# Kernel optimization log

Measured on AMD Instinct MI355X. Metric: run time of the kernel, lower is better.

## Reference

```python
import jax, jax.numpy as jnp
import numpy as np

STRIDES = (4.0, 8.0, 16.0, 32.0)
IMG = 1024.0


def setup_inputs() -> dict:
    key = jax.random.key(0)
    ks = jax.random.split(key, 10)
    N, P = 512, 128
    feat0 = jax.random.normal(ks[0], (2, 256, 256, 256), jnp.float32)
    feat1 = jax.random.normal(ks[1], (2, 256, 128, 128), jnp.float32)
    feat2 = jax.random.normal(ks[2], (2, 256, 64, 64), jnp.float32)
    feat3 = jax.random.normal(ks[3], (2, 256, 32, 32), jnp.float32)
    b = jax.random.randint(ks[4], (N,), 0, 2).astype(jnp.float32)
    x1 = jax.random.uniform(ks[5], (N,)) * 512.0
    y1 = jax.random.uniform(ks[6], (N,)) * 512.0
    w = 16.0 + jax.random.uniform(ks[7], (N,)) * 496.0
    h = 16.0 + jax.random.uniform(ks[8], (N,)) * 496.0
    rois = jnp.stack([b, x1, y1, x1 + w, y1 + h], axis=1)  # [N,5]
    points = jax.random.uniform(ks[9], (N, P, 2), jnp.float32)  # rel coords in [0,1]
    return {"feat0": feat0, "feat1": feat1, "feat2": feat2, "feat3": feat3,
            "rois": rois, "points": points}


def _sample_level(feat, coords, batch_idx, stride):
    # feat: [B,C,H,W]; coords: [N,P,2] absolute image (x,y); -> [N,C,P]
    B, C, H, W = feat.shape
    # grid_sample align_corners=False: pixel coord = img_coord/stride - 0.5
    px = coords[..., 0] / stride - 0.5
    py = coords[..., 1] / stride - 0.5
    x0 = jnp.floor(px)
    y0 = jnp.floor(py)
    wx = px - x0  # weight of x0+1
    wy = py - y0
    x0i = x0.astype(jnp.int32)
    y0i = y0.astype(jnp.int32)

    def gather(yi, xi):
        valid = (xi >= 0) & (xi < W) & (yi >= 0) & (yi < H)  # zeros padding
        xc = jnp.clip(xi, 0, W - 1)
        yc = jnp.clip(yi, 0, H - 1)
        v = feat[batch_idx[:, None], :, yc, xc]  # [N,P,C]
        return v * valid[..., None].astype(feat.dtype)

    v00 = gather(y0i, x0i)
    v01 = gather(y0i, x0i + 1)
    v10 = gather(y0i + 1, x0i)
    v11 = gather(y0i + 1, x0i + 1)
    wx = wx[..., None]
    wy = wy[..., None]
    out = (v00 * (1 - wx) * (1 - wy) + v01 * wx * (1 - wy)
           + v10 * (1 - wx) * wy + v11 * wx * wy)  # [N,P,C]
    return out.transpose(0, 2, 1)  # [N,C,P]


def reference(feat0, feat1, feat2, feat3, rois, points):
    batch_idx = rois[:, 0].astype(jnp.int32)  # [N]
    xy1 = rois[:, 1:3]  # [N,2]
    xy2 = rois[:, 3:5]
    # roi_point2img_coord: rel point -> absolute image coordinate
    coords = xy1[:, None, :] + points * (xy2 - xy1)[:, None, :]  # [N,P,2]
    feats = (feat0, feat1, feat2, feat3)
    per_level = [_sample_level(f, coords, batch_idx, s) for f, s in zip(feats, STRIDES)]
    return jnp.concatenate(per_level, axis=1)  # [N, sum(C)=1024, P]
```

## Files before the change

kernel.cpp:

```cpp
#include <hip/hip_runtime.h>
#include <hip/hip_bf16.h>

#define N_ROIS 512
#define P_PTS  128
#define C_CH   256
#define TILE_P 32

#define L0_OFS 0
#define L1_OFS 33554432u
#define L2_OFS 41943040u
#define L3_OFS 44040192u
#define WS_ELEMS_NEEDED 44564480u

__device__ inline unsigned pack_bf16x2(float lo, float hi) {
    __hip_bfloat162 h = __float22bfloat162_rn(make_float2(lo, hi));
    unsigned r;
    __builtin_memcpy(&r, &h, 4);
    return r;
}

__global__ __launch_bounds__(256) void transpose_all_bf16(
    const float* __restrict__ f0, const float* __restrict__ f1,
    const float* __restrict__ f2, const float* __restrict__ f3,
    unsigned short* __restrict__ ws)
{
    const float* in; unsigned short* outp; int HW, pt;
    const int px = blockIdx.x;
    if (px < 2048)      { in = f0; outp = ws + L0_OFS; HW = 65536; pt = px; }
    else if (px < 2560) { in = f1; outp = ws + L1_OFS; HW = 16384; pt = px - 2048; }
    else if (px < 2688) { in = f2; outp = ws + L2_OFS; HW = 4096;  pt = px - 2560; }
    else                { in = f3; outp = ws + L3_OFS; HW = 1024;  pt = px - 2688; }

    __shared__ float tile[32][33];
    const int pix0 = pt * 32;
    const int c0   = blockIdx.y * 32;
    const int b    = blockIdx.z;
    in   += (size_t)b * C_CH * HW;
    outp += (size_t)b * C_CH * HW;
    const int tx = threadIdx.x;
    const int ty = threadIdx.y;

    #pragma unroll
    for (int i = 0; i < 32; i += 8)
        tile[ty + i][tx] = in[(size_t)(c0 + ty + i) * HW + pix0 + tx];
    __syncthreads();

    const int tid2 = ty * 32 + tx;
    const int wpix = tid2 >> 3;
    const int wq   = tid2 & 7;
    uint2 pk;
    pk.x = pack_bf16x2(tile[wq * 4 + 0][wpix], tile[wq * 4 + 1][wpix]);
    pk.y = pack_bf16x2(tile[wq * 4 + 2][wpix], tile[wq * 4 + 3][wpix]);
    *((uint2*)(outp + (size_t)(pix0 + wpix) * C_CH + c0 + wq * 4)) = pk;
}

__global__ __launch_bounds__(256) void mpe_sample_nhwc_bf16_v4(
    const unsigned short* __restrict__ fT,
    const float* __restrict__ rois, const float* __restrict__ points,
    float* __restrict__ out)
{
    const int blk = blockIdx.x;
    const int n   = blk >> 2;
    const int lvl = blk & 3;

    int H; float inv_stride; size_t lofs;
    if      (lvl == 0) { H = 256; inv_stride = 0.25f;    lofs = L0_OFS; }
    else if (lvl == 1) { H = 128; inv_stride = 0.125f;   lofs = L1_OFS; }
    else if (lvl == 2) { H = 64;  inv_stride = 0.0625f;  lofs = L2_OFS; }
    else               { H = 32;  inv_stride = 0.03125f; lofs = L3_OFS; }
    const int W  = H;
    const int HW = H * W;
    const unsigned short* feat = fT + lofs;

    __shared__ int   s_off[P_PTS][4];
    __shared__ float s_w[P_PTS][4];
    __shared__ float s_t[TILE_P][C_CH];

    const int tid = threadIdx.x;

    if (tid < P_PTS) {
        const int p = tid;
        const float bx = rois[n * 5 + 0];
        const float x1 = rois[n * 5 + 1];
        const float y1 = rois[n * 5 + 2];
        const float x2 = rois[n * 5 + 3];
        const float y2 = rois[n * 5 + 4];
        const float ptx = points[(n * P_PTS + p) * 2 + 0];
        const float pty = points[(n * P_PTS + p) * 2 + 1];

        const float cx = x1 + ptx * (x2 - x1);
        const float cy = y1 + pty * (y2 - y1);
        const float px = cx * inv_stride - 0.5f;
        const float py = cy * inv_stride - 0.5f;
        const float x0f = floorf(px);
        const float y0f = floorf(py);
        const float wx = px - x0f;
        const float wy = py - y0f;
        const int x0 = (int)x0f;
        const int y0 = (int)y0f;
        const int base = (int)bx * HW;

        #pragma unroll
        for (int k = 0; k < 4; ++k) {
            const int xi = x0 + (k & 1);
            const int yi = y0 + (k >> 1);
            const bool valid = (xi >= 0) & (xi < W) & (yi >= 0) & (yi < H);
            const int xc = min(max(xi, 0), W - 1);
            const int yc = min(max(yi, 0), H - 1);
            const float wk = ((k & 1) ? wx : 1.0f - wx) *
                             ((k >> 1) ? wy : 1.0f - wy);
            s_off[p][k] = base + yc * W + xc;
            s_w[p][k]   = valid ? wk : 0.0f;
        }
    }
    __syncthreads();

    const int wave = tid >> 6;
    const int lane = tid & 63;

    uint2 v[8][4];
    #pragma unroll
    for (int j = 0; j < 8; ++j) {
        const int pp = wave * 8 + j;
        #pragma unroll
        for (int k = 0; k < 4; ++k)
            v[j][k] = *((const uint2*)(feat + (size_t)s_off[pp][k] * C_CH) + lane);
    }

    for (int tile = 0; tile < P_PTS / TILE_P; ++tile) {
        const int pbase = tile * TILE_P + wave * 8;

        #pragma unroll
        for (int j = 0; j < 8; ++j) {
            const int pp = pbase + j;
            float4 a = make_float4(0.f, 0.f, 0.f, 0.f);
            #pragma unroll
            for (int k = 0; k < 4; ++k) {
                const float wk = s_w[pp][k];
                a.x = fmaf(__uint_as_float(v[j][k].x << 16),         wk, a.x);
                a.y = fmaf(__uint_as_float(v[j][k].x & 0xffff0000u), wk, a.y);
                a.z = fmaf(__uint_as_float(v[j][k].y << 16),         wk, a.z);
                a.w = fmaf(__uint_as_float(v[j][k].y & 0xffff0000u), wk, a.w);
            }
            *((float4*)&s_t[wave * 8 + j][lane * 4]) = a;
        }
        __syncthreads();

        if (tile < P_PTS / TILE_P - 1) {
            #pragma unroll
            for (int j = 0; j < 8; ++j) {
                const int pp = pbase + TILE_P + j;
                #pragma unroll
                for (int k = 0; k < 4; ++k)
                    v[j][k] = *((const uint2*)(feat + (size_t)s_off[pp][k] * C_CH) + lane);
            }
        }

        float* ob = out + ((size_t)n * 1024 + (size_t)lvl * 256 + tid) * P_PTS
                        + tile * TILE_P;
        #pragma unroll
        for (int i = 0; i < TILE_P / 4; ++i) {
            float4 o = make_float4(s_t[i * 4 + 0][tid], s_t[i * 4 + 1][tid],
                                   s_t[i * 4 + 2][tid], s_t[i * 4 + 3][tid]);
            *((float4*)(ob + i * 4)) = o;
        }
        __syncthreads();
    }
}

__global__ __launch_bounds__(256) void mpe_sample_nchw(
    const float* __restrict__ feat0, const float* __restrict__ feat1,
    const float* __restrict__ feat2, const float* __restrict__ feat3,
    const float* __restrict__ rois,  const float* __restrict__ points,
    float* __restrict__ out)
{
    const int blk = blockIdx.x;
    const int n   = blk >> 2;
    const int lvl = blk & 3;

    const float* feat;
    int H; float inv_stride;
    if      (lvl == 0) { feat = feat0; H = 256; inv_stride = 0.25f;    }
    else if (lvl == 1) { feat = feat1; H = 128; inv_stride = 0.125f;   }
    else if (lvl == 2) { feat = feat2; H = 64;  inv_stride = 0.0625f;  }
    else               { feat = feat3; H = 32;  inv_stride = 0.03125f; }
    const int W  = H;
    const int HW = H * W;

    __shared__ int   s_off[4][P_PTS];
    __shared__ float s_w[4][P_PTS];
    const int tid = threadIdx.x;

    if (tid < P_PTS) {
        const int p = tid;
        const float bx = rois[n * 5 + 0];
        const float x1 = rois[n * 5 + 1];
        const float y1 = rois[n * 5 + 2];
        const float x2 = rois[n * 5 + 3];
        const float y2 = rois[n * 5 + 4];
        const float ptx = points[(n * P_PTS + p) * 2 + 0];
        const float pty = points[(n * P_PTS + p) * 2 + 1];
        const float cx = x1 + ptx * (x2 - x1);
        const float cy = y1 + pty * (y2 - y1);
        const float px = cx * inv_stride - 0.5f;
        const float py = cy * inv_stride - 0.5f;
        const float x0f = floorf(px);
        const float y0f = floorf(py);
        const float wx = px - x0f;
        const float wy = py - y0f;
        const int x0 = (int)x0f;
        const int y0 = (int)y0f;
        const int base = (int)bx * C_CH * HW;
        #pragma unroll
        for (int k = 0; k < 4; ++k) {
            const int xi = x0 + (k & 1);
            const int yi = y0 + (k >> 1);
            const bool valid = (xi >= 0) & (xi < W) & (yi >= 0) & (yi < H);
            const int xc = min(max(xi, 0), W - 1);
            const int yc = min(max(yi, 0), H - 1);
            const float wk = ((k & 1) ? wx : 1.0f - wx) *
                             ((k >> 1) ? wy : 1.0f - wy);
            s_off[k][p] = base + yc * W + xc;
            s_w[k][p]   = valid ? wk : 0.0f;
        }
    }
    __syncthreads();

    const int p  = tid & (P_PTS - 1);
    const int c0 = tid >> 7;
    const int   off0 = s_off[0][p], off1 = s_off[1][p],
                off2 = s_off[2][p], off3 = s_off[3][p];
    const float w0 = s_w[0][p], w1 = s_w[1][p],
                w2 = s_w[2][p], w3 = s_w[3][p];
    const float* p0 = feat + off0 + c0 * HW;
    const float* p1 = feat + off1 + c0 * HW;
    const float* p2 = feat + off2 + c0 * HW;
    const float* p3 = feat + off3 + c0 * HW;
    float* po = out + ((size_t)n * 1024 + (size_t)lvl * 256 + c0) * P_PTS + p;
    const int step = 2 * HW;
    #pragma unroll 4
    for (int pass = 0; pass < C_CH / 2; ++pass) {
        *po = p0[0] * w0 + p1[0] * w1 + p2[0] * w2 + p3[0] * w3;
        p0 += step; p1 += step; p2 += step; p3 += step;
        po += 2 * P_PTS;
    }
}

extern "C" void kernel_launch(void* const* d_in, const int* in_sizes, int n_in,
                              void* d_out, int out_size, void* d_ws, size_t ws_size,
                              hipStream_t stream) {
    const float* feat0  = (const float*)d_in[0];
    const float* feat1  = (const float*)d_in[1];
    const float* feat2  = (const float*)d_in[2];
    const float* feat3  = (const float*)d_in[3];
    const float* rois   = (const float*)d_in[4];
    const float* points = (const float*)d_in[5];
    float* out = (float*)d_out;

    if (ws_size >= (size_t)WS_ELEMS_NEEDED * 2u) {
        unsigned short* fT = (unsigned short*)d_ws;
        transpose_all_bf16<<<dim3(2720, 8, 2), dim3(32, 8), 0, stream>>>(
            feat0, feat1, feat2, feat3, fT);
        mpe_sample_nhwc_bf16_v4<<<dim3(N_ROIS * 4), dim3(256), 0, stream>>>(
            fT, rois, points, out);
    } else {
        mpe_sample_nchw<<<dim3(N_ROIS * 4), dim3(256), 0, stream>>>(
            feat0, feat1, feat2, feat3, rois, points, out);
    }
}
```

Measured before the change: 212.4 us.

## Double-buffer sampling tile in bf16 LDS, halve tile, use nontemporal output stores

```diff
diff --git a/kernel.cpp b/kernel.cpp
--- a/kernel.cpp
+++ b/kernel.cpp
@@ -4,7 +4,8 @@
 #define N_ROIS 512
 #define P_PTS  128
 #define C_CH   256
-#define TILE_P 32
+#define TILE_P 16
+#define N_TILES (P_PTS / TILE_P)
 
 #define L0_OFS 0
 #define L1_OFS 33554432u
@@ -12,11 +13,16 @@
 #define L3_OFS 44040192u
 #define WS_ELEMS_NEEDED 44564480u
 
+typedef float f32x4 __attribute__((ext_vector_type(4)));
+
 __device__ inline unsigned pack_bf16x2(float lo, float hi) {
     __hip_bfloat162 h = __float22bfloat162_rn(make_float2(lo, hi));
     unsigned r;
     __builtin_memcpy(&r, &h, 4);
     return r;
+}
+__device__ inline float bf16_to_f32(unsigned short u) {
+    return __uint_as_float(((unsigned)u) << 16);
 }
 
 __global__ __launch_bounds__(256) void transpose_all_bf16(
@@ -54,7 +60,7 @@
     *((uint2*)(outp + (size_t)(pix0 + wpix) * C_CH + c0 + wq * 4)) = pk;
 }
 
-__global__ __launch_bounds__(256) void mpe_sample_nhwc_bf16_v4(
+__global__ __launch_bounds__(256, 6) void mpe_sample_v5(
     const unsigned short* __restrict__ fT,
     const float* __restrict__ rois, const float* __restrict__ points,
     float* __restrict__ out)
@@ -72,9 +78,9 @@
     const int HW = H * W;
     const unsigned short* feat = fT + lofs;
 
-    __shared__ int   s_off[P_PTS][4];
-    __shared__ float s_w[P_PTS][4];
-    __shared__ float s_t[TILE_P][C_CH];
+    __shared__ int4   s_off4[P_PTS];
+    __shared__ float4 s_w4[P_PTS];
+    __shared__ unsigned short s_t[2][TILE_P][C_CH];
 
     const int tid = threadIdx.x;
 
@@ -100,6 +106,7 @@
         const int y0 = (int)y0f;
         const int base = (int)bx * HW;
 
+        int   o[4]; float w[4];
         #pragma unroll
         for (int k = 0; k < 4; ++k) {
             const int xi = x0 + (k & 1);
@@ -109,62 +116,86 @@
             const int yc = min(max(yi, 0), H - 1);
             const float wk = ((k & 1) ? wx : 1.0f - wx) *
                              ((k >> 1) ? wy : 1.0f - wy);
-            s_off[p][k] = base + yc * W + xc;
-            s_w[p][k]   = valid ? wk : 0.0f;
-        }
+            o[k] = base + yc * W + xc;
+            w[k] = valid ? wk : 0.0f;
+        }
+        s_off4[p] = make_int4(o[0], o[1], o[2], o[3]);
+        s_w4[p]   = make_float4(w[0], w[1], w[2], w[3]);
     }
     __syncthreads();
 
     const int wave = tid >> 6;
     const int lane = tid & 63;
 
-    uint2 v[8][4];
+    uint2 v[4][4];
     #pragma unroll
-    for (int j = 0; j < 8; ++j) {
-        const int pp = wave * 8 + j;
+    for (int j = 0; j < 4; ++j) {
+        const int4 o = s_off4[wave * 4 + j];
+        v[j][0] = *((const uint2*)(feat + (size_t)o.x * C_CH) + lane);
+        v[j][1] = *((const uint2*)(feat + (size_t)o.y * C_CH) + lane);
+        v[j][2] = *((const uint2*)(feat + (size_t)o.z * C_CH) + lane);
+        v[j][3] = *((const uint2*)(feat + (size_t)o.w * C_CH) + lane);
+    }
+
+    float* const ob_base = out + ((size_t)n * 1024 + (size_t)lvl * 256 + tid) * P_PTS;
+
+    for (int t = 0; t < N_TILES; ++t) {
+        const int b = t & 1;
+        const int pbase = t * TILE_P + wave * 4;
+
         #pragma unroll
-        for (int k = 0; k < 4; ++k)
-            v[j][k] = *((const uint2*)(feat + (size_t)s_off[pp][k] * C_CH) + lane);
-    }
-
-    for (int tile = 0; tile < P_PTS / TILE_P; ++tile) {
-        const int pbase = tile * TILE_P + wave * 8;
-
+        for (int j = 0; j < 4; ++j) {
+            const float4 wj = s_w4[pbase + j];
+            float4 a;
+            a.x = fmaf(bf16_to_f32((unsigned short)(v[j][0].x & 0xffffu)), wj.x, 0.f);
+            a.y = fmaf(bf16_to_f32((unsigned short)(v[j][0].x >> 16)),     wj.x, 0.f);
+            a.z = fmaf(bf16_to_f32((unsigned short)(v[j][0].y & 0xffffu)), wj.x, 0.f);
+            a.w = fmaf(bf16_to_f32((unsigned short)(v[j][0].y >> 16)),     wj.x, 0.f);
+            const float wk1 = wj.y, wk2 = wj.z, wk3 = wj.w;
+            a.x = fmaf(bf16_to_f32((unsigned short)(v[j][1].x & 0xffffu)), wk1, a.x);
+            a.y = fmaf(bf16_to_f32((unsigned short)(v[j][1].x >> 16)),     wk1, a.y);
+            a.z = fmaf(bf16_to_f32((unsigned short)(v[j][1].y & 0xffffu)), wk1, a.z);
+            a.w = fmaf(bf16_to_f32((unsigned short)(v[j][1].y >> 16)),     wk1, a.w);
+            a.x = fmaf(bf16_to_f32((unsigned short)(v[j][2].x & 0xffffu)), wk2, a.x);
+            a.y = fmaf(bf16_to_f32((unsigned short)(v[j][2].x >> 16)),     wk2, a.y);
+            a.z = fmaf(bf16_to_f32((unsigned short)(v[j][2].y & 0xffffu)), wk2, a.z);
+            a.w = fmaf(bf16_to_f32((unsigned short)(v[j][2].y >> 16)),     wk2, a.w);
+            a.x = fmaf(bf16_to_f32((unsigned short)(v[j][3].x & 0xffffu)), wk3, a.x);
+            a.y = fmaf(bf16_to_f32((unsigned short)(v[j][3].x >> 16)),     wk3, a.y);
+            a.z = fmaf(bf16_to_f32((unsigned short)(v[j][3].y & 0xffffu)), wk3, a.z);
+            a.w = fmaf(bf16_to_f32((unsigned short)(v[j][3].y >> 16)),     wk3, a.w);
+            uint2 pk;
+            pk.x = pack_bf16x2(a.x, a.y);
+            pk.y = pack_bf16x2(a.z, a.w);
+            *((uint2*)&s_t[b][wave * 4 + j][lane * 4]) = pk;
+        }
+
+        if (t < N_TILES - 1) {
+            const int pnext = pbase + TILE_P;
+            #pragma unroll
+            for (int j = 0; j < 4; ++j) {
+                const int4 o = s_off4[pnext + j];
+                v[j][0] = *((const uint2*)(feat + (size_t)o.x * C_CH) + lane);
+                v[j][1] = *((const uint2*)(feat + (size_t)o.y * C_CH) + lane);
+                v[j][2] = *((const uint2*)(feat + (size_t)o.z * C_CH) + lane);
+                v[j][3] = *((const uint2*)(feat + (size_t)o.w * C_CH) + lane);
+            }
+        }
+
+        asm volatile("s_waitcnt lgkmcnt(0)" ::: "memory");
+        __builtin_amdgcn_s_barrier();
+        __builtin_amdgcn_sched_barrier(0);
+
+        float* ob = ob_base + t * TILE_P;
         #pragma unroll
-        for (int j = 0; j < 8; ++j) {
-            const int pp = pbase + j;
-            float4 a = make_float4(0.f, 0.f, 0.f, 0.f);
-            #pragma unroll
-            for (int k = 0; k < 4; ++k) {
-                const float wk = s_w[pp][k];
-                a.x = fmaf(__uint_as_float(v[j][k].x << 16),         wk, a.x);
-                a.y = fmaf(__uint_as_float(v[j][k].x & 0xffff0000u), wk, a.y);
-                a.z = fmaf(__uint_as_float(v[j][k].y << 16),         wk, a.z);
-                a.w = fmaf(__uint_as_float(v[j][k].y & 0xffff0000u), wk, a.w);
-            }
-            *((float4*)&s_t[wave * 8 + j][lane * 4]) = a;
-        }
-        __syncthreads();
-
-        if (tile < P_PTS / TILE_P - 1) {
-            #pragma unroll
-            for (int j = 0; j < 8; ++j) {
-                const int pp = pbase + TILE_P + j;
-                #pragma unroll
-                for (int k = 0; k < 4; ++k)
-                    v[j][k] = *((const uint2*)(feat + (size_t)s_off[pp][k] * C_CH) + lane);
-            }
-        }
-
-        float* ob = out + ((size_t)n * 1024 + (size_t)lvl * 256 + tid) * P_PTS
-                        + tile * TILE_P;
-        #pragma unroll
-        for (int i = 0; i < TILE_P / 4; ++i) {
-            float4 o = make_float4(s_t[i * 4 + 0][tid], s_t[i * 4 + 1][tid],
-                                   s_t[i * 4 + 2][tid], s_t[i * 4 + 3][tid]);
-            *((float4*)(ob + i * 4)) = o;
-        }
-        __syncthreads();
+        for (int i4 = 0; i4 < TILE_P / 4; ++i4) {
+            f32x4 oq;
+            oq.x = bf16_to_f32(s_t[b][i4 * 4 + 0][tid]);
+            oq.y = bf16_to_f32(s_t[b][i4 * 4 + 1][tid]);
+            oq.z = bf16_to_f32(s_t[b][i4 * 4 + 2][tid]);
+            oq.w = bf16_to_f32(s_t[b][i4 * 4 + 3][tid]);
+            __builtin_nontemporal_store(oq, (f32x4*)(ob + i4 * 4));
+        }
     }
 }
 
@@ -261,7 +292,7 @@
         unsigned short* fT = (unsigned short*)d_ws;
         transpose_all_bf16<<<dim3(2720, 8, 2), dim3(32, 8), 0, stream>>>(
             feat0, feat1, feat2, feat3, fT);
-        mpe_sample_nhwc_bf16_v4<<<dim3(N_ROIS * 4), dim3(256), 0, stream>>>(
+        mpe_sample_v5<<<dim3(N_ROIS * 4), dim3(256), 0, stream>>>(
             fT, rois, points, out);
     } else {
         mpe_sample_nchw<<<dim3(N_ROIS * 4), dim3(256), 0, stream>>>(
```

Result: slower. 591.4 us (+178.4%).
